# Performance work log

Measured on AMD Instinct MI355X. Metric: run time of the kernel, lower is better.

Reference implementation:

```python
import jax, jax.numpy as jnp
import numpy as np

PRECISION = 127.0

def _pwb_quantize(t):
    # Pulse-width binary mapping: clip to [-1, 1] (layer constraint) and
    # quantize to `precision` discrete levels, as PWBMapper realizes weights.
    t = jnp.clip(t, -1.0, 1.0)
    return jnp.round(t * PRECISION) / PRECISION

def setup_inputs() -> dict:
    key = jax.random.key(0)
    k1, k2, k3 = jax.random.split(key, 3)
    B, DIN, DOUT = 4096, 2048, 2048
    x = jax.random.normal(k1, (B, DIN), dtype=jnp.float32)
    # tf.random_normal_initializer default stddev = 0.05
    W = jax.random.normal(k2, (DIN, DOUT), dtype=jnp.float32) * 0.05
    b = jax.random.normal(k3, (DOUT,), dtype=jnp.float32) * 0.05
    return {"x": x, "W": W, "b": b}

def reference(x, W, b):
    # Fused equivalent of the per-sample / per-neuron Python loops:
    # each neuron's PWB step is a dot product with the quantized weight
    # column; the bias neuron adds the quantized bias. Then activation.
    Wq = _pwb_quantize(W)            # [DIN, DOUT]
    bq = _pwb_quantize(b)            # [DOUT]
    y = jnp.einsum('bi,io->bo', x, Wq) + bq
    return jax.nn.relu(y)
```

## Files before the change

### kernel.cpp

```cpp
#include <hip/hip_runtime.h>
#include <hip/hip_bf16.h>
#include <stdint.h>


typedef __attribute__((ext_vector_type(4))) int i32x4;

#define BM 128
#define BN 128
#define BK 64

__device__ __forceinline__ float pwb_clip(float w) {
    return fminf(fmaxf(w, -1.f), 1.f);
}

__device__ __forceinline__ void gl16(const int8_t* g, int8_t* l) {
    __builtin_amdgcn_global_load_lds(
        (const __attribute__((address_space(1))) void*)(g),
        (__attribute__((address_space(3))) void*)(l),
        16, 0, 0);
}

#define WAIT_VM6   asm volatile("s_waitcnt vmcnt(6)" ::: "memory");
#define WAIT_VM4   asm volatile("s_waitcnt vmcnt(4)" ::: "memory");
#define WAIT_VM2   asm volatile("s_waitcnt vmcnt(2)" ::: "memory");
#define WAIT_VM0   asm volatile("s_waitcnt vmcnt(0)" ::: "memory");
#define BAR()      __builtin_amdgcn_s_barrier();

__global__ void pwb_prep(const float* __restrict__ x, const float* __restrict__ W,
                         int8_t* __restrict__ xq, int8_t* __restrict__ Wq,
                         float* __restrict__ scales, int DIN, int DOUT, int xblocks) {
    __shared__ __align__(16) float smem[4 * 2048];
    const int tid = threadIdx.x;
    const size_t KB = (size_t)(DIN >> 6) << 10;

    if ((int)blockIdx.x < xblocks) {
        const int wv = tid >> 6, l = tid & 63;
        const int row = blockIdx.x * 4 + wv;
        const float4* xr = (const float4*)(x + (size_t)row * DIN);
        float* xs = smem + wv * 2048;
        const int J = DIN >> 8;
        float m = 0.f;
        for (int j = 0; j < J; ++j) {
            float4 v = xr[j * 64 + l];
            *(float4*)&xs[j * 256 + l * 4] = v;
            m = fmaxf(m, fmaxf(fmaxf(fabsf(v.x), fabsf(v.y)),
                               fmaxf(fabsf(v.z), fabsf(v.w))));
        }
#pragma unroll
        for (int d = 1; d < 64; d <<= 1) m = fmaxf(m, __shfl_xor(m, d));
        const float r = (m > 0.f) ? 127.f / m : 0.f;
        if (l == 0) scales[row] = m / 16129.f;
        int8_t* orow_ = xq + (size_t)(row >> 4) * KB + (row & 15) * 64;
        for (int j = 0; j < J; ++j) {
            float4 v = *(const float4*)&xs[j * 256 + l * 4];
            int q0 = (int)rintf(v.x * r), q1 = (int)rintf(v.y * r);
            int q2 = (int)rintf(v.z * r), q3 = (int)rintf(v.w * r);
            uint32_t u = (uint32_t)(q0 & 255) | ((uint32_t)(q1 & 255) << 8) |
                         ((uint32_t)(q2 & 255) << 16) | ((uint32_t)(q3 & 255) << 24);
            *(uint32_t*)(orow_ + (size_t)(j * 4 + (l >> 4)) * 1024 + (l & 15) * 4) = u;
        }
    } else {
        int8_t* tq = (int8_t*)smem;
        const int wb = blockIdx.x - xblocks;
        const int gw = DOUT >> 6;
        const int c0 = (wb % gw) * 64;
        const int r0 = (wb / gw) * 64;
        const int kl = tid >> 4;
        const int nc = (tid & 15) * 4;
#pragma unroll
        for (int i = 0; i < 4; ++i) {
            int k = r0 + kl + i * 16;
            float4 wv = *(const float4*)&W[(size_t)k * DOUT + c0 + nc];
            tq[(nc + 0) * 72 + kl + i * 16] = (int8_t)rintf(pwb_clip(wv.x) * 127.f);
            tq[(nc + 1) * 72 + kl + i * 16] = (int8_t)rintf(pwb_clip(wv.y) * 127.f);
            tq[(nc + 2) * 72 + kl + i * 16] = (int8_t)rintf(pwb_clip(wv.z) * 127.f);
            tq[(nc + 3) * 72 + kl + i * 16] = (int8_t)rintf(pwb_clip(wv.w) * 127.f);
        }
        __syncthreads();
        const int nl = tid >> 2, cc = (tid & 3) * 16;
        uint4 u;
        u.x = *(const uint32_t*)&tq[nl * 72 + cc + 0];
        u.y = *(const uint32_t*)&tq[nl * 72 + cc + 4];
        u.z = *(const uint32_t*)&tq[nl * 72 + cc + 8];
        u.w = *(const uint32_t*)&tq[nl * 72 + cc + 12];
        const int n = c0 + nl;
        *(uint4*)(Wq + (size_t)(n >> 4) * KB +
                  (size_t)(r0 >> 6) * 1024 + (n & 15) * 64 + cc) = u;
    }
}

__global__ __launch_bounds__(256, 2) void pwb_gemmq(
    const int8_t* __restrict__ A,
    const int8_t* __restrict__ Bt,
    const float* __restrict__ scales,
    const float* __restrict__ b,
    float* __restrict__ C,
    int M, int N, int K, int GN, int nwg) {
    __shared__ __align__(16) int8_t lA[4][BM * BK];

    const int tid = threadIdx.x;
    const int w   = tid >> 6;
    const int l   = tid & 63;
    const int lr  = l & 15;
    const int lk  = l >> 4;

    const int bid = blockIdx.x;
    const int q = nwg >> 3, r = nwg & 7;
    const int xcd = bid & 7, lin = bid >> 3;
    const int wgid = (xcd < r ? xcd * (q + 1) : r * (q + 1) + (xcd - r) * q) + lin;
    const int tm = wgid / GN, tn = wgid % GN;
    const size_t brow = (size_t)tm * BM, bcol = (size_t)tn * BN;

    const int wm = (w >> 1) * 64;
    const int wn = (w & 1) * 64;

    const int KT = K >> 6;
    const size_t KB = (size_t)KT << 10;

    const int8_t* gA[2];
#pragma unroll
    for (int i = 0; i < 2; ++i) {
        int s = tid + 256 * i;
        int c = s & 63, rr = c >> 2, sl = c & 3;
        int gc = rr * 4 + (sl ^ ((rr >> 1) & 3));
        gA[i] = A + (size_t)((brow >> 4) + (s >> 6)) * KB + gc * 16;
    }
    const int8_t* pB = Bt + (size_t)((bcol + wn) >> 4) * KB + lr * 64 + lk * 16;
    const int offA = (wm >> 4) * 1024 + lr * 64 + ((lk ^ ((lr >> 1) & 3)) << 4);

    i32x4 acc[4][4] = {};
    i32x4 bS0[4], bS1[4], afr[4];

#define STAGE(buf, t)                                                   \
    gl16(gA[0] + (size_t)(t) * 1024, &lA[buf][tid * 16]);               \
    gl16(gA[1] + (size_t)(t) * 1024, &lA[buf][(tid + 256) * 16]);

#define LOADB(set, t)                                                   \
    _Pragma("unroll") for (int nj = 0; nj < 4; ++nj)                    \
        set[nj] = *(const i32x4*)(pB + (size_t)nj * KB + (size_t)(t) * 1024);

#define LOADA(buf)                                                      \
    _Pragma("unroll") for (int mi = 0; mi < 4; ++mi)                    \
        afr[mi] = *(const i32x4*)&lA[buf][offA + mi * 1024];

#define MFMA16(fb)                                                      \
    __builtin_amdgcn_s_setprio(1);                                      \
    _Pragma("unroll") for (int mi = 0; mi < 4; ++mi)                    \
    _Pragma("unroll") for (int nj = 0; nj < 4; ++nj)                    \
        acc[mi][nj] = __builtin_amdgcn_mfma_i32_16x16x64_i8(            \
            afr[mi], fb[nj], acc[mi][nj], 0, 0, 0);                     \
    __builtin_amdgcn_s_setprio(0);

    STAGE(0, 0)
    LOADB(bS0, 0)
    STAGE(1, 1)
    WAIT_VM2
    BAR();

    const int T = KT;
    for (int it = 0; it < (T - 2) / 2; ++it) {
        const int t0 = 2 * it;
        LOADB(bS1, t0 + 1)
        STAGE((t0 + 2) & 3, t0 + 2)
        LOADA(t0 & 3)
        WAIT_VM6
        BAR();
        MFMA16(bS0)
        LOADB(bS0, t0 + 2)
        STAGE((t0 + 3) & 3, t0 + 3)
        LOADA((t0 + 1) & 3)
        WAIT_VM6
        BAR();
        MFMA16(bS1)
    }
    LOADB(bS1, T - 1)
    LOADA((T - 2) & 3)
    WAIT_VM4
    BAR();
    MFMA16(bS0)
    WAIT_VM0
    LOADA((T - 1) & 3)
    MFMA16(bS1)

    float bias[4];
#pragma unroll
    for (int nj = 0; nj < 4; ++nj) {
        float bv = b[bcol + wn + nj * 16 + lr];
        bias[nj] = rintf(pwb_clip(bv) * 127.f) * (1.f / 127.f);
    }

    const size_t orow = brow + wm + lk * 4;
    const size_t ocol = bcol + wn + lr;
    float4 scl[4];
#pragma unroll
    for (int mi = 0; mi < 4; ++mi)
        scl[mi] = *(const float4*)&scales[orow + mi * 16];

#pragma unroll
    for (int mi = 0; mi < 4; ++mi) {
        const float s0_ = scl[mi].x, s1_ = scl[mi].y, s2_ = scl[mi].z, s3_ = scl[mi].w;
#pragma unroll
        for (int nj = 0; nj < 4; ++nj) {
            float v0 = fmaf((float)acc[mi][nj][0], s0_, bias[nj]);
            float v1 = fmaf((float)acc[mi][nj][1], s1_, bias[nj]);
            float v2 = fmaf((float)acc[mi][nj][2], s2_, bias[nj]);
            float v3 = fmaf((float)acc[mi][nj][3], s3_, bias[nj]);
            float* cp = &C[(orow + mi * 16) * N + (ocol + nj * 16)];
            cp[0 * N] = fmaxf(v0, 0.f);
            cp[1 * N] = fmaxf(v1, 0.f);
            cp[2 * N] = fmaxf(v2, 0.f);
            cp[3 * N] = fmaxf(v3, 0.f);
        }
    }
#undef STAGE
#undef LOADB
#undef LOADA
#undef MFMA16
}

__global__ void pwb_fallback(const float* __restrict__ x, const float* __restrict__ W,
                             const float* __restrict__ b, float* __restrict__ out,
                             int M, int N, int K) {
    __shared__ float sA[16][17];
    __shared__ float sB[16][17];
    int tx = threadIdx.x, ty = threadIdx.y;
    int row = blockIdx.y * 16 + ty;
    int col = blockIdx.x * 16 + tx;
    float acc = 0.f;
    for (int kt = 0; kt < K; kt += 16) {
        sA[ty][tx] = (row < M && kt + tx < K) ? x[(size_t)row * K + kt + tx] : 0.f;
        float w = (kt + ty < K && col < N) ? W[(size_t)(kt + ty) * N + col] : 0.f;
        sB[ty][tx] = rintf(pwb_clip(w) * 127.f) * (1.f / 127.f);
        __syncthreads();
#pragma unroll
        for (int kk = 0; kk < 16; ++kk) acc += sA[ty][kk] * sB[kk][tx];
        __syncthreads();
    }
    if (row < M && col < N) {
        float v = acc + rintf(pwb_clip(b[col]) * 127.f) * (1.f / 127.f);
        out[(size_t)row * N + col] = fmaxf(v, 0.f);
    }
}

extern "C" void kernel_launch(void* const* d_in, const int* in_sizes, int n_in,
                              void* d_out, int out_size, void* d_ws, size_t ws_size,
                              hipStream_t stream) {
    const float* x = (const float*)d_in[0];
    const float* W = (const float*)d_in[1];
    const float* b = (const float*)d_in[2];
    float* out = (float*)d_out;

    const int DOUT = in_sizes[2];
    const int DIN  = in_sizes[1] / DOUT;
    const int M    = in_sizes[0] / DIN;

    size_t need = (size_t)M * DIN + (size_t)DIN * DOUT + (size_t)M * 4;
    const int T = DIN / 64;
    bool fast = (M % BM == 0) && (M % 4 == 0) && (DOUT % BN == 0) &&
                (DIN % 256 == 0) && (DIN <= 2048) && (T >= 4) && ((T & 1) == 0) &&
                (ws_size >= need);

    if (fast) {
        int8_t* xq = (int8_t*)d_ws;
        int8_t* Wq = xq + (size_t)M * DIN;
        float* scales = (float*)(Wq + (size_t)DIN * DOUT);

        const int xblocks = M / 4;
        const int wblocks = (DIN / 64) * (DOUT / 64);
        pwb_prep<<<xblocks + wblocks, 256, 0, stream>>>(x, W, xq, Wq, scales,
                                                        DIN, DOUT, xblocks);

        const int GM = M / BM, GN = DOUT / BN, nwg = GM * GN;
        pwb_gemmq<<<nwg, 256, 0, stream>>>(xq, Wq, scales, b, out, M, DOUT, DIN, GN, nwg);
    } else {
        dim3 g((DOUT + 15) / 16, (M + 15) / 16), blk(16, 16);
        pwb_fallback<<<g, blk, 0, stream>>>(x, W, b, out, M, DOUT, DIN);
    }
}
```

Baseline: 40.48 us.

## Remap warp tiling to 128x32 per wave, sharing A-fragments across full tile rows

Each of the four waves now covers all 128 rows and a 32-column slice, instead of a 2x2 arrangement of 64x64 sub-tiles. Per K-step a wave reads 8 A fragments from LDS and only 2 B fragments from global memory, so the direct global B loads are halved. The vmcnt wait counts are lowered to match. The cost is more LDS reads per wave and a different register-use profile, which could change how well the global load latency is hidden.

```diff
diff --git a/kernel.cpp b/kernel.cpp
--- a/kernel.cpp
+++ b/kernel.cpp
@@ -20,7 +20,6 @@
         16, 0, 0);
 }
 
-#define WAIT_VM6   asm volatile("s_waitcnt vmcnt(6)" ::: "memory");
 #define WAIT_VM4   asm volatile("s_waitcnt vmcnt(4)" ::: "memory");
 #define WAIT_VM2   asm volatile("s_waitcnt vmcnt(2)" ::: "memory");
 #define WAIT_VM0   asm volatile("s_waitcnt vmcnt(0)" ::: "memory");
@@ -111,9 +110,6 @@
     const int tm = wgid / GN, tn = wgid % GN;
     const size_t brow = (size_t)tm * BM, bcol = (size_t)tn * BN;
 
-    const int wm = (w >> 1) * 64;
-    const int wn = (w & 1) * 64;
-
     const int KT = K >> 6;
     const size_t KB = (size_t)KT << 10;
 
@@ -125,28 +121,28 @@
         int gc = rr * 4 + (sl ^ ((rr >> 1) & 3));
         gA[i] = A + (size_t)((brow >> 4) + (s >> 6)) * KB + gc * 16;
     }
-    const int8_t* pB = Bt + (size_t)((bcol + wn) >> 4) * KB + lr * 64 + lk * 16;
-    const int offA = (wm >> 4) * 1024 + lr * 64 + ((lk ^ ((lr >> 1) & 3)) << 4);
-
-    i32x4 acc[4][4] = {};
-    i32x4 bS0[4], bS1[4], afr[4];
+    const int8_t* pB = Bt + (size_t)((bcol >> 4) + w * 2) * KB + lr * 64 + lk * 16;
+    const int offA = lr * 64 + ((lk ^ ((lr >> 1) & 3)) << 4);
+
+    i32x4 acc[8][2] = {};
+    i32x4 bS0[2], bS1[2], afr[8];
 
 #define STAGE(buf, t)                                                   \
     gl16(gA[0] + (size_t)(t) * 1024, &lA[buf][tid * 16]);               \
     gl16(gA[1] + (size_t)(t) * 1024, &lA[buf][(tid + 256) * 16]);
 
 #define LOADB(set, t)                                                   \
-    _Pragma("unroll") for (int nj = 0; nj < 4; ++nj)                    \
+    _Pragma("unroll") for (int nj = 0; nj < 2; ++nj)                    \
         set[nj] = *(const i32x4*)(pB + (size_t)nj * KB + (size_t)(t) * 1024);
 
 #define LOADA(buf)                                                      \
-    _Pragma("unroll") for (int mi = 0; mi < 4; ++mi)                    \
+    _Pragma("unroll") for (int mi = 0; mi < 8; ++mi)                    \
         afr[mi] = *(const i32x4*)&lA[buf][offA + mi * 1024];
 
 #define MFMA16(fb)                                                      \
     __builtin_amdgcn_s_setprio(1);                                      \
-    _Pragma("unroll") for (int mi = 0; mi < 4; ++mi)                    \
-    _Pragma("unroll") for (int nj = 0; nj < 4; ++nj)                    \
+    _Pragma("unroll") for (int mi = 0; mi < 8; ++mi)                    \
+    _Pragma("unroll") for (int nj = 0; nj < 2; ++nj)                    \
         acc[mi][nj] = __builtin_amdgcn_mfma_i32_16x16x64_i8(            \
             afr[mi], fb[nj], acc[mi][nj], 0, 0, 0);                     \
     __builtin_amdgcn_s_setprio(0);
@@ -163,48 +159,43 @@
         LOADB(bS1, t0 + 1)
         STAGE((t0 + 2) & 3, t0 + 2)
         LOADA(t0 & 3)
-        WAIT_VM6
+        WAIT_VM4
         BAR();
         MFMA16(bS0)
         LOADB(bS0, t0 + 2)
         STAGE((t0 + 3) & 3, t0 + 3)
         LOADA((t0 + 1) & 3)
-        WAIT_VM6
+        WAIT_VM4
         BAR();
         MFMA16(bS1)
     }
     LOADB(bS1, T - 1)
     LOADA((T - 2) & 3)
-    WAIT_VM4
+    WAIT_VM2
     BAR();
     MFMA16(bS0)
     WAIT_VM0
     LOADA((T - 1) & 3)
     MFMA16(bS1)
 
-    float bias[4];
-#pragma unroll
-    for (int nj = 0; nj < 4; ++nj) {
-        float bv = b[bcol + wn + nj * 16 + lr];
+    float bias[2];
+#pragma unroll
+    for (int nj = 0; nj < 2; ++nj) {
+        float bv = b[bcol + w * 32 + nj * 16 + lr];
         bias[nj] = rintf(pwb_clip(bv) * 127.f) * (1.f / 127.f);
     }
 
-    const size_t orow = brow + wm + lk * 4;
-    const size_t ocol = bcol + wn + lr;
-    float4 scl[4];
-#pragma unroll
-    for (int mi = 0; mi < 4; ++mi)
-        scl[mi] = *(const float4*)&scales[orow + mi * 16];
-
-#pragma unroll
-    for (int mi = 0; mi < 4; ++mi) {
-        const float s0_ = scl[mi].x, s1_ = scl[mi].y, s2_ = scl[mi].z, s3_ = scl[mi].w;
-#pragma unroll
-        for (int nj = 0; nj < 4; ++nj) {
-            float v0 = fmaf((float)acc[mi][nj][0], s0_, bias[nj]);
-            float v1 = fmaf((float)acc[mi][nj][1], s1_, bias[nj]);
-            float v2 = fmaf((float)acc[mi][nj][2], s2_, bias[nj]);
-            float v3 = fmaf((float)acc[mi][nj][3], s3_, bias[nj]);
+    const size_t orow = brow + lk * 4;
+    const size_t ocol = bcol + w * 32 + lr;
+#pragma unroll
+    for (int mi = 0; mi < 8; ++mi) {
+        float4 scl = *(const float4*)&scales[orow + mi * 16];
+#pragma unroll
+        for (int nj = 0; nj < 2; ++nj) {
+            float v0 = fmaf((float)acc[mi][nj][0], scl.x, bias[nj]);
+            float v1 = fmaf((float)acc[mi][nj][1], scl.y, bias[nj]);
+            float v2 = fmaf((float)acc[mi][nj][2], scl.z, bias[nj]);
+            float v3 = fmaf((float)acc[mi][nj][3], scl.w, bias[nj]);
             float* cp = &C[(orow + mi * 16) * N + (ocol + nj * 16)];
             cp[0 * N] = fmaxf(v0, 0.f);
             cp[1 * N] = fmaxf(v1, 0.f);
```

Result: faster. 35.88 us, median of 2 (-11.4%).
